# Kernel tuning notes

Measured on AMD Instinct MI355X. Metric: run time of the kernel, lower is better.

## Reference

```python
import jax, jax.numpy as jnp
import numpy as np

N_NODES, N_EDGES = 100000, 400000
D_NODE, D_EDGE, N_COND, N_ROUNDS = 128, 64, 2, 3


def gru_cell(x, h, Wih, Whh, bih, bhh):
    # Standard torch.nn.GRUCell math. x: [N, D] input, h: [N, D] hidden.
    gi = x @ Wih.T + bih            # [N, 3D]
    gh = h @ Whh.T + bhh            # [N, 3D]
    ir, iz, inn = jnp.split(gi, 3, axis=-1)
    hr, hz, hn = jnp.split(gh, 3, axis=-1)
    r = jax.nn.sigmoid(ir + hr)
    z = jax.nn.sigmoid(iz + hz)
    n = jnp.tanh(inn + r * hn)
    return (1.0 - z) * n + z * h


def setup_inputs() -> dict:
    key = jax.random.key(0)
    ks = jax.random.split(key, 10)
    scale = jnp.float32(0.05)
    d_in = 2 * D_NODE + D_EDGE + N_COND  # 322, matches enc_U Linear in_features
    h = jax.random.normal(ks[0], (N_NODES, D_NODE), jnp.float32)
    e = jax.random.normal(ks[1], (N_EDGES, D_EDGE), jnp.float32)
    src = jax.random.randint(ks[2], (N_EDGES,), 0, N_NODES)
    dst = jax.random.randint(ks[3], (N_EDGES,), 0, N_NODES)
    cond = jax.random.normal(ks[4], (N_COND,), jnp.float32)
    U_W = jax.random.normal(ks[5], (N_ROUNDS, D_NODE, d_in), jnp.float32) * scale
    U_b = jnp.zeros((N_ROUNDS, D_NODE), jnp.float32)
    Wih = jax.random.normal(ks[6], (N_ROUNDS, 3 * D_NODE, D_NODE), jnp.float32) * scale
    Whh = jax.random.normal(ks[7], (N_ROUNDS, 3 * D_NODE, D_NODE), jnp.float32) * scale
    bih = jnp.zeros((N_ROUNDS, 3 * D_NODE), jnp.float32)
    bhh = jnp.zeros((N_ROUNDS, 3 * D_NODE), jnp.float32)
    return dict(h=h, e=e, src=src, dst=dst, cond=cond,
                U_W=U_W, U_b=U_b, Wih=Wih, Whh=Whh, bih=bih, bhh=bhh)


def reference(h, e, src, dst, cond, U_W, U_b, Wih, Whh, bih, bhh):
    # GGM encode(): 3 rounds of gather-concat-Linear(enc_U)-segment_sum-GRUCell(enc_C).
    n_nodes = h.shape[0]
    n_edges = e.shape[0]
    cond_e = jnp.broadcast_to(cond, (n_edges, cond.shape[0]))
    for k in range(U_W.shape[0]):
        # per-edge message input: [h_v, h_w, e_vw, condition] -> [E, 2D+DE+NC]
        x = jnp.concatenate([h[dst], h[src], e, cond_e], axis=-1)
        msg = x @ U_W[k].T + U_b[k]                              # [E, D]
        agg = jax.ops.segment_sum(msg, dst, num_segments=n_nodes)  # [N, D]
        h = gru_cell(agg, h, Wih[k], Whh[k], bih[k], bhh[k])
    return h
```

## Files before the change

kernel.cpp:

```cpp
#include <hip/hip_runtime.h>
#include <hip/hip_bf16.h>
#include <hip/hip_fp16.h>


#define D_NODE 128
#define D_EDGE 64
#define D_IN   322
#define GRU3   384
#define ROWS_BLK 256
#define PA_STRIDE 328
#define PB_STRIDE 136

typedef _Float16 f16x8 __attribute__((ext_vector_type(8)));
typedef _Float16 f16x4 __attribute__((ext_vector_type(4)));
typedef _Float16 f16x2 __attribute__((ext_vector_type(2)));
typedef float    f32x4 __attribute__((ext_vector_type(4)));
typedef unsigned short u16x8 __attribute__((ext_vector_type(8)));

__device__ __forceinline__ f16x8 as_f16x8(u16x8 v) { return __builtin_bit_cast(f16x8, v); }
__device__ __forceinline__ float sigm_(float x) { return 1.f / (1.f + __expf(-x)); }
__device__ __forceinline__ float tanh_(float x) { return 1.f - 2.f / (__expf(2.f * x) + 1.f); }

__global__ void hist_k(const int* __restrict__ dst, int* __restrict__ cnt, int E) {
    int t = blockIdx.x * 256 + threadIdx.x;
    if (t < E) atomicAdd(&cnt[dst[t]], 1);
}

__global__ __launch_bounds__(256) void scan1_k(const int* __restrict__ cnt, int* __restrict__ row_ptr,
                                               int* __restrict__ blk_sums, int N) {
    __shared__ int s[256];
    const int t = threadIdx.x;
    const int base = blockIdx.x * 1024 + t * 4;
    int v0 = (base + 0 < N) ? cnt[base + 0] : 0;
    int v1 = (base + 1 < N) ? cnt[base + 1] : 0;
    int v2 = (base + 2 < N) ? cnt[base + 2] : 0;
    int v3 = (base + 3 < N) ? cnt[base + 3] : 0;
    const int tot = v0 + v1 + v2 + v3;
    s[t] = tot;
    __syncthreads();
    for (int off = 1; off < 256; off <<= 1) {
        int u = (t >= off) ? s[t - off] : 0;
        __syncthreads();
        s[t] += u;
        __syncthreads();
    }
    const int excl = s[t] - tot;
    if (base + 0 < N) row_ptr[base + 0] = excl;
    if (base + 1 < N) row_ptr[base + 1] = excl + v0;
    if (base + 2 < N) row_ptr[base + 2] = excl + v0 + v1;
    if (base + 3 < N) row_ptr[base + 3] = excl + v0 + v1 + v2;
    if (t == 255) blk_sums[blockIdx.x] = s[255];
}

__global__ __launch_bounds__(256) void scan2_k(int* __restrict__ blk_sums, int NB,
                                               int* __restrict__ row_ptr, int N, int E) {
    __shared__ int s[256];
    const int t = threadIdx.x;
    const int v = (t < NB) ? blk_sums[t] : 0;
    s[t] = v;
    __syncthreads();
    for (int off = 1; off < 256; off <<= 1) {
        int u = (t >= off) ? s[t - off] : 0;
        __syncthreads();
        s[t] += u;
        __syncthreads();
    }
    if (t < NB) blk_sums[t] = s[t] - v;
    if (t == 0) row_ptr[N] = E;
}

__global__ __launch_bounds__(256) void scan3_k(int* __restrict__ row_ptr, int* __restrict__ cursor,
                                               const int* __restrict__ blk_sums, int N) {
    const int off = blk_sums[blockIdx.x];
    const int base = blockIdx.x * 1024 + threadIdx.x * 4;
#pragma unroll
    for (int j = 0; j < 4; ++j) {
        const int i = base + j;
        if (i < N) {
            const int v = row_ptr[i] + off;
            row_ptr[i] = v;
            cursor[i] = v;
        }
    }
}

__global__ void scatter_k(const int* __restrict__ src, const int* __restrict__ dst,
                          int* __restrict__ cursor, int* __restrict__ csr_src,
                          int* __restrict__ csr_eid, int E) {
    int t = blockIdx.x * 256 + threadIdx.x;
    if (t < E) {
        int d = dst[t];
        int pos = atomicAdd(&cursor[d], 1);
        csr_src[pos] = src[t];
        csr_eid[pos] = t;
    }
}

__global__ __launch_bounds__(320) void cvt_uwp_k(const float* __restrict__ in, _Float16* __restrict__ out) {
    const int row = blockIdx.x;
    const int t = threadIdx.x;
    out[(size_t)row * 320 + t] = (_Float16)in[(size_t)row * D_IN + t];
}

__global__ void cvt_f32_k(const float* __restrict__ in, _Float16* __restrict__ out, int n) {
    int t = blockIdx.x * 256 + threadIdx.x;
    if (t < n) out[t] = (_Float16)in[t];
}

__global__ void cvt4_k(const float* __restrict__ in, _Float16* __restrict__ out, int n4) {
    int t = blockIdx.x * 256 + threadIdx.x;
    if (t < n4) {
        const f32x4 v = ((const f32x4*)in)[t];
        f16x4 r;
        r[0] = (_Float16)v[0]; r[1] = (_Float16)v[1];
        r[2] = (_Float16)v[2]; r[3] = (_Float16)v[3];
        ((f16x4*)out)[t] = r;
    }
}

__global__ void cvt_out_k(const _Float16* __restrict__ in, float* __restrict__ out, int n4) {
    int t = blockIdx.x * 256 + threadIdx.x;
    if (t < n4) {
        const f16x4 v = ((const f16x4*)in)[t];
        f32x4 r;
        r[0] = (float)v[0]; r[1] = (float)v[1];
        r[2] = (float)v[2]; r[3] = (float)v[3];
        ((f32x4*)out)[t] = r;
    }
}

__global__ void compute_c_k(const float* __restrict__ UW, const float* __restrict__ Ub,
                            const float* __restrict__ cond, float* __restrict__ cvec) {
    int t = threadIdx.x;
    if (t < 3 * D_NODE) {
        int k = t >> 7, i = t & 127;
        const float* u = UW + (size_t)k * D_NODE * D_IN + (size_t)i * D_IN + 320;
        cvec[t] = u[0] * cond[0] + u[1] * cond[1] + Ub[k * D_NODE + i];
    }
}

__global__ __launch_bounds__(256) void gather_e_k(const float* __restrict__ e,
                                                  const int* __restrict__ row_ptr,
                                                  const int* __restrict__ csr_eid,
                                                  _Float16* __restrict__ S_e, int N) {
    const int wave = threadIdx.x >> 6, lane = threadIdx.x & 63;
    const int n = blockIdx.x * 4 + wave;
    if (n >= N) return;
    const int p0 = row_ptr[n], p1 = row_ptr[n + 1];
    float a = 0.f, b = 0.f, c = 0.f, d = 0.f;
    int p = p0;
    for (; p + 3 < p1; p += 4) {
        const int e0 = csr_eid[p], e1 = csr_eid[p + 1], e2 = csr_eid[p + 2], e3 = csr_eid[p + 3];
        a += e[(size_t)e0 * D_EDGE + lane];
        b += e[(size_t)e1 * D_EDGE + lane];
        c += e[(size_t)e2 * D_EDGE + lane];
        d += e[(size_t)e3 * D_EDGE + lane];
    }
    for (; p < p1; ++p) a += e[(size_t)csr_eid[p] * D_EDGE + lane];
    S_e[(size_t)n * D_EDGE + lane] = (_Float16)((a + b) + (c + d));
}

__global__ __launch_bounds__(256) void gather_e16_k(const _Float16* __restrict__ e16,
                                                    const int* __restrict__ row_ptr,
                                                    const int* __restrict__ csr_eid,
                                                    _Float16* __restrict__ S_e, int N) {
    const int wave = threadIdx.x >> 6, lane = threadIdx.x & 63;
    const int half = lane >> 5, ln = lane & 31;
    const int n = blockIdx.x * 8 + wave * 2 + half;
    if (n >= N) return;
    const unsigned* ep = (const unsigned*)e16;
    const int p0 = row_ptr[n], p1 = row_ptr[n + 1];
    float a0 = 0.f, a1 = 0.f, b0 = 0.f, b1 = 0.f;
    float c0 = 0.f, c1 = 0.f, d0 = 0.f, d1 = 0.f;
    int p = p0;
    for (; p + 3 < p1; p += 4) {
        const int e0 = csr_eid[p], e1 = csr_eid[p + 1], e2 = csr_eid[p + 2], e3 = csr_eid[p + 3];
        const f16x2 v0 = __builtin_bit_cast(f16x2, ep[(size_t)e0 * 32 + ln]);
        const f16x2 v1 = __builtin_bit_cast(f16x2, ep[(size_t)e1 * 32 + ln]);
        const f16x2 v2 = __builtin_bit_cast(f16x2, ep[(size_t)e2 * 32 + ln]);
        const f16x2 v3 = __builtin_bit_cast(f16x2, ep[(size_t)e3 * 32 + ln]);
        a0 += (float)v0[0]; a1 += (float)v0[1];
        b0 += (float)v1[0]; b1 += (float)v1[1];
        c0 += (float)v2[0]; c1 += (float)v2[1];
        d0 += (float)v3[0]; d1 += (float)v3[1];
    }
    for (; p < p1; ++p) {
        const f16x2 v = __builtin_bit_cast(f16x2, ep[(size_t)csr_eid[p] * 32 + ln]);
        a0 += (float)v[0]; a1 += (float)v[1];
    }
    f16x2 r;
    r[0] = (_Float16)((a0 + b0) + (c0 + d0));
    r[1] = (_Float16)((a1 + b1) + (c1 + d1));
    ((unsigned*)S_e)[(size_t)n * 32 + ln] = __builtin_bit_cast(unsigned, r);
}

__global__ __launch_bounds__(256) void gather_h_k(const _Float16* __restrict__ h16,
                                                  const int* __restrict__ row_ptr,
                                                  const int* __restrict__ csr_src,
                                                  _Float16* __restrict__ S_h, int N) {
    const int wave = threadIdx.x >> 6, lane = threadIdx.x & 63;
    const int half = lane >> 5, ln = lane & 31;
    const int n = blockIdx.x * 8 + wave * 2 + half;
    if (n >= N) return;
    const uint2* hp = (const uint2*)h16;
    const int p0 = row_ptr[n], p1 = row_ptr[n + 1];
    float aA[4] = {0.f,0.f,0.f,0.f}, aB[4] = {0.f,0.f,0.f,0.f};
    float aC[4] = {0.f,0.f,0.f,0.f}, aD[4] = {0.f,0.f,0.f,0.f};
    int p = p0;
    for (; p + 3 < p1; p += 4) {
        const int s0 = csr_src[p], s1 = csr_src[p + 1], s2 = csr_src[p + 2], s3 = csr_src[p + 3];
        const f16x4 v0 = __builtin_bit_cast(f16x4, hp[(size_t)s0 * 32 + ln]);
        const f16x4 v1 = __builtin_bit_cast(f16x4, hp[(size_t)s1 * 32 + ln]);
        const f16x4 v2 = __builtin_bit_cast(f16x4, hp[(size_t)s2 * 32 + ln]);
        const f16x4 v3 = __builtin_bit_cast(f16x4, hp[(size_t)s3 * 32 + ln]);
#pragma unroll
        for (int j = 0; j < 4; ++j) {
            aA[j] += (float)v0[j]; aB[j] += (float)v1[j];
            aC[j] += (float)v2[j]; aD[j] += (float)v3[j];
        }
    }
    for (; p < p1; ++p) {
        const f16x4 v = __builtin_bit_cast(f16x4, hp[(size_t)csr_src[p] * 32 + ln]);
#pragma unroll
        for (int j = 0; j < 4; ++j) aA[j] += (float)v[j];
    }
    f16x4 r;
#pragma unroll
    for (int j = 0; j < 4; ++j) r[j] = (_Float16)((aA[j] + aB[j]) + (aC[j] + aD[j]));
    ((uint2*)S_h)[(size_t)n * 32 + ln] = __builtin_bit_cast(uint2, r);
}

__global__ __launch_bounds__(512, 2) void agg_k(
    const _Float16* __restrict__ h16,
    const _Float16* __restrict__ S_h,
    const _Float16* __restrict__ S_e,
    const int* __restrict__ row_ptr,
    const float* __restrict__ cvec,
    const _Float16* __restrict__ UWp,
    _Float16* __restrict__ agg,
    int N) {
    __shared__ __align__(16) _Float16 pbuf[2][16 * PA_STRIDE];

    const int tid  = threadIdx.x;
    const int wave = tid >> 6;
    const int lane = tid & 63;
    const int l15  = lane & 15;
    const int lg   = lane >> 4;
    const int rbase = blockIdx.x * ROWS_BLK + wave * 32;

    const unsigned short* hp  = (const unsigned short*)h16;
    const unsigned short* shp = (const unsigned short*)S_h;
    const unsigned short* sep = (const unsigned short*)S_e;
    const unsigned short* uwp = (const unsigned short*)UWp;

    f16x8 a_h[2][4], a_sh[2][4], a_se[2][2];
#pragma unroll
    for (int m = 0; m < 2; ++m) {
        const int arow = min(rbase + m * 16 + l15, N - 1);
#pragma unroll
        for (int kb = 0; kb < 4; ++kb) {
            a_h[m][kb]  = as_f16x8(*(const u16x8*)(hp  + (size_t)arow * D_NODE + kb * 32 + lg * 8));
            a_sh[m][kb] = as_f16x8(*(const u16x8*)(shp + (size_t)arow * D_NODE + kb * 32 + lg * 8));
        }
#pragma unroll
        for (int kb = 0; kb < 2; ++kb)
            a_se[m][kb] = as_f16x8(*(const u16x8*)(sep + (size_t)arow * D_EDGE + kb * 32 + lg * 8));
    }
    float degv[2][4];
#pragma unroll
    for (int m = 0; m < 2; ++m)
#pragma unroll
        for (int i = 0; i < 4; ++i) {
            const int n = min(rbase + m * 16 + lg * 4 + i, N - 1);
            degv[m][i] = (float)(row_ptr[n + 1] - row_ptr[n]);
        }

    u16x8 pr0, pr1;
    auto load_panel = [&](int nb) {
        const int c0 = tid, c1 = 512 + tid;
        pr0 = *(const u16x8*)(uwp + (size_t)(nb * 16 + c0 / 40) * 320 + (c0 % 40) * 8);
        if (c1 < 640)
            pr1 = *(const u16x8*)(uwp + (size_t)(nb * 16 + c1 / 40) * 320 + (c1 % 40) * 8);
    };
    auto write_panel = [&](int b) {
        const int c0 = tid, c1 = 512 + tid;
        *(u16x8*)&pbuf[b][(c0 / 40) * PA_STRIDE + (c0 % 40) * 8] = pr0;
        if (c1 < 640)
            *(u16x8*)&pbuf[b][(c1 / 40) * PA_STRIDE + (c1 % 40) * 8] = pr1;
    };

    load_panel(0);
    write_panel(0);
    __syncthreads();

#pragma unroll 1
    for (int nb = 0; nb < 8; ++nb) {
        if (nb < 7) load_panel(nb + 1);
        const _Float16* bp = pbuf[nb & 1];
        f32x4 acc1[2] = {{0.f,0.f,0.f,0.f},{0.f,0.f,0.f,0.f}};
        f32x4 acc2[2] = {{0.f,0.f,0.f,0.f},{0.f,0.f,0.f,0.f}};
#pragma unroll
        for (int kb = 0; kb < 10; ++kb) {
            f16x8 b = as_f16x8(*(const u16x8*)&bp[l15 * PA_STRIDE + kb * 32 + lg * 8]);
            if (kb < 4) {
                acc1[0] = __builtin_amdgcn_mfma_f32_16x16x32_f16(a_h[0][kb], b, acc1[0], 0, 0, 0);
                acc1[1] = __builtin_amdgcn_mfma_f32_16x16x32_f16(a_h[1][kb], b, acc1[1], 0, 0, 0);
            } else if (kb < 8) {
                acc2[0] = __builtin_amdgcn_mfma_f32_16x16x32_f16(a_sh[0][kb-4], b, acc2[0], 0, 0, 0);
                acc2[1] = __builtin_amdgcn_mfma_f32_16x16x32_f16(a_sh[1][kb-4], b, acc2[1], 0, 0, 0);
            } else {
                acc2[0] = __builtin_amdgcn_mfma_f32_16x16x32_f16(a_se[0][kb-8], b, acc2[0], 0, 0, 0);
                acc2[1] = __builtin_amdgcn_mfma_f32_16x16x32_f16(a_se[1][kb-8], b, acc2[1], 0, 0, 0);
            }
        }
        const float cv = cvec[nb * 16 + l15];
#pragma unroll
        for (int m = 0; m < 2; ++m)
#pragma unroll
            for (int i = 0; i < 4; ++i) {
                const int n = rbase + m * 16 + lg * 4 + i;
                if (n < N)
                    agg[(size_t)n * D_NODE + nb * 16 + l15] =
                        (_Float16)(degv[m][i] * (acc1[m][i] + cv) + acc2[m][i]);
            }
        if (nb < 7) write_panel((nb + 1) & 1);
        __syncthreads();
    }
}

__global__ __launch_bounds__(512, 2) void gru_k(
    _Float16* __restrict__ h16,
    const _Float16* __restrict__ agg,
    const _Float16* __restrict__ Wihh,
    const _Float16* __restrict__ Whhh,
    const float* __restrict__ bih,
    const float* __restrict__ bhh,
    int N) {
    __shared__ __align__(16) _Float16 pbuf[2][96 * PB_STRIDE];

    const int tid  = threadIdx.x;
    const int wave = tid >> 6;
    const int lane = tid & 63;
    const int l15  = lane & 15;
    const int lg   = lane >> 4;
    const int rbase = blockIdx.x * ROWS_BLK + wave * 32;

    const unsigned short* hp  = (const unsigned short*)h16;
    const unsigned short* agp = (const unsigned short*)agg;
    const unsigned short* wih = (const unsigned short*)Wihh;
    const unsigned short* whh = (const unsigned short*)Whhh;

    f16x8 a_ag[2][4], a_h[2][4];
#pragma unroll
    for (int m = 0; m < 2; ++m) {
        const int arow = min(rbase + m * 16 + l15, N - 1);
#pragma unroll
        for (int kb = 0; kb < 4; ++kb) {
            a_ag[m][kb] = as_f16x8(*(const u16x8*)(agp + (size_t)arow * D_NODE + kb * 32 + lg * 8));
            a_h[m][kb]  = as_f16x8(*(const u16x8*)(hp  + (size_t)arow * D_NODE + kb * 32 + lg * 8));
        }
    }

    u16x8 pr[3];
    auto load_panel = [&](int nb) {
#pragma unroll
        for (int r = 0; r < 3; ++r) {
            const int c = r * 512 + tid;
            const int row = c >> 4;
            const int off = (c & 15) * 8;
            const int gate = row >> 4;
            const int col = nb * 16 + (row & 15) + (gate % 3) * D_NODE;
            const unsigned short* mat = (gate < 3) ? wih : whh;
            pr[r] = *(const u16x8*)(mat + (size_t)col * D_NODE + off);
        }
    };
    auto write_panel = [&](int b) {
#pragma unroll
        for (int r = 0; r < 3; ++r) {
            const int c = r * 512 + tid;
            const int row = c >> 4;
            const int off = (c & 15) * 8;
            *(u16x8*)&pbuf[b][row * PB_STRIDE + off] = pr[r];
        }
    };

    load_panel(0);
    write_panel(0);
    __syncthreads();

#pragma unroll 1
    for (int nb = 0; nb < 8; ++nb) {
        if (nb < 7) load_panel(nb + 1);
        const int d = nb * 16 + l15;
        float hv[2][4];
#pragma unroll
        for (int m = 0; m < 2; ++m)
#pragma unroll
            for (int i = 0; i < 4; ++i) {
                const int n = min(rbase + m * 16 + lg * 4 + i, N - 1);
                hv[m][i] = (float)h16[(size_t)n * D_NODE + d];
            }
        const float bir = bih[d],       biz = bih[128 + d], bin = bih[256 + d];
        const float bhr = bhh[d],       bhz = bhh[128 + d], bhn = bhh[256 + d];

        const _Float16* bp = pbuf[nb & 1];
        f32x4 air[2] = {{0.f,0.f,0.f,0.f},{0.f,0.f,0.f,0.f}};
        f32x4 aiz[2] = {{0.f,0.f,0.f,0.f},{0.f,0.f,0.f,0.f}};
        f32x4 ain_[2] = {{0.f,0.f,0.f,0.f},{0.f,0.f,0.f,0.f}};
        f32x4 ahr[2] = {{0.f,0.f,0.f,0.f},{0.f,0.f,0.f,0.f}};
        f32x4 ahz[2] = {{0.f,0.f,0.f,0.f},{0.f,0.f,0.f,0.f}};
        f32x4 ahn[2] = {{0.f,0.f,0.f,0.f},{0.f,0.f,0.f,0.f}};
#pragma unroll
        for (int kb = 0; kb < 4; ++kb) {
            const int ko = kb * 32 + lg * 8;
            f16x8 b;
            b = as_f16x8(*(const u16x8*)&bp[(0 * 16 + l15) * PB_STRIDE + ko]);
            air[0] = __builtin_amdgcn_mfma_f32_16x16x32_f16(a_ag[0][kb], b, air[0], 0, 0, 0);
            air[1] = __builtin_amdgcn_mfma_f32_16x16x32_f16(a_ag[1][kb], b, air[1], 0, 0, 0);
            b = as_f16x8(*(const u16x8*)&bp[(1 * 16 + l15) * PB_STRIDE + ko]);
            aiz[0] = __builtin_amdgcn_mfma_f32_16x16x32_f16(a_ag[0][kb], b, aiz[0], 0, 0, 0);
            aiz[1] = __builtin_amdgcn_mfma_f32_16x16x32_f16(a_ag[1][kb], b, aiz[1], 0, 0, 0);
            b = as_f16x8(*(const u16x8*)&bp[(2 * 16 + l15) * PB_STRIDE + ko]);
            ain_[0] = __builtin_amdgcn_mfma_f32_16x16x32_f16(a_ag[0][kb], b, ain_[0], 0, 0, 0);
            ain_[1] = __builtin_amdgcn_mfma_f32_16x16x32_f16(a_ag[1][kb], b, ain_[1], 0, 0, 0);
            b = as_f16x8(*(const u16x8*)&bp[(3 * 16 + l15) * PB_STRIDE + ko]);
            ahr[0] = __builtin_amdgcn_mfma_f32_16x16x32_f16(a_h[0][kb], b, ahr[0], 0, 0, 0);
            ahr[1] = __builtin_amdgcn_mfma_f32_16x16x32_f16(a_h[1][kb], b, ahr[1], 0, 0, 0);
            b = as_f16x8(*(const u16x8*)&bp[(4 * 16 + l15) * PB_STRIDE + ko]);
            ahz[0] = __builtin_amdgcn_mfma_f32_16x16x32_f16(a_h[0][kb], b, ahz[0], 0, 0, 0);
            ahz[1] = __builtin_amdgcn_mfma_f32_16x16x32_f16(a_h[1][kb], b, ahz[1], 0, 0, 0);
            b = as_f16x8(*(const u16x8*)&bp[(5 * 16 + l15) * PB_STRIDE + ko]);
            ahn[0] = __builtin_amdgcn_mfma_f32_16x16x32_f16(a_h[0][kb], b, ahn[0], 0, 0, 0);
            ahn[1] = __builtin_amdgcn_mfma_f32_16x16x32_f16(a_h[1][kb], b, ahn[1], 0, 0, 0);
        }
#pragma unroll
        for (int m = 0; m < 2; ++m)
#pragma unroll
            for (int i = 0; i < 4; ++i) {
                const int n = rbase + m * 16 + lg * 4 + i;
                if (n < N) {
                    const float r  = sigm_(air[m][i] + bir + ahr[m][i] + bhr);
                    const float z  = sigm_(aiz[m][i] + biz + ahz[m][i] + bhz);
                    const float nn = tanh_(ain_[m][i] + bin + r * (ahn[m][i] + bhn));
                    h16[(size_t)n * D_NODE + d] = (_Float16)((1.f - z) * nn + z * hv[m][i]);
                }
            }
        if (nb < 7) write_panel((nb + 1) & 1);
        __syncthreads();
    }
}

extern "C" void kernel_launch(void* const* d_in, const int* in_sizes, int n_in,
                              void* d_out, int out_size, void* d_ws, size_t ws_size,
                              hipStream_t stream) {
    const float* h0   = (const float*)d_in[0];
    const float* e    = (const float*)d_in[1];
    const int*   src  = (const int*)d_in[2];
    const int*   dst  = (const int*)d_in[3];
    const float* cond = (const float*)d_in[4];
    const float* UW   = (const float*)d_in[5];
    const float* Ub   = (const float*)d_in[6];
    const float* Wih  = (const float*)d_in[7];
    const float* Whh  = (const float*)d_in[8];
    const float* bih  = (const float*)d_in[9];
    const float* bhh  = (const float*)d_in[10];

    const int N = in_sizes[0] / D_NODE;
    const int E = in_sizes[2];
    const int NB = (N + 1023) / 1024;
    const int NT = (N + ROWS_BLK - 1) / ROWS_BLK;

    char* wsb = (char*)d_ws;
    size_t off = 0;
    auto carve = [&](size_t bytes) -> char* {
        char* p = wsb + off;
        off = (off + bytes + 255) & ~(size_t)255;
        return p;
    };
    int*   cnt      = (int*)carve((size_t)N * 4);
    int*   row_ptr  = (int*)carve(((size_t)N + 1) * 4);
    int*   cursor   = (int*)carve((size_t)N * 4);
    int*   csr_src  = (int*)carve((size_t)E * 4);
    int*   csr_eid  = (int*)carve((size_t)E * 4);
    int*   blk_sums = (int*)carve(256 * 4);
    float* cvec     = (float*)carve(3 * D_NODE * 4);
    _Float16* S_e  = (_Float16*)carve((size_t)N * D_EDGE * 2);
    _Float16* S_h  = (_Float16*)carve((size_t)N * D_NODE * 2);
    _Float16* aggb = (_Float16*)carve((size_t)N * D_NODE * 2);
    _Float16* h16  = (_Float16*)carve((size_t)N * D_NODE * 2);
    _Float16* UWp  = (_Float16*)carve((size_t)3 * D_NODE * 320 * 2);
    _Float16* Wihh = (_Float16*)carve((size_t)3 * GRU3 * D_NODE * 2);
    _Float16* Whhh = (_Float16*)carve((size_t)3 * GRU3 * D_NODE * 2);
    const size_t e16_bytes = (size_t)E * D_EDGE * 2;
    _Float16* e16 = nullptr;
    if (off + e16_bytes + 256 <= ws_size) e16 = (_Float16*)carve(e16_bytes);
    (void)n_in; (void)out_size;

    hipMemsetAsync(cnt, 0, (size_t)N * 4, stream);
    hist_k<<<(E + 255) / 256, 256, 0, stream>>>(dst, cnt, E);
    scan1_k<<<NB, 256, 0, stream>>>(cnt, row_ptr, blk_sums, N);
    scan2_k<<<1, 256, 0, stream>>>(blk_sums, NB, row_ptr, N, E);
    scan3_k<<<NB, 256, 0, stream>>>(row_ptr, cursor, blk_sums, N);
    scatter_k<<<(E + 255) / 256, 256, 0, stream>>>(src, dst, cursor, csr_src, csr_eid, E);
    compute_c_k<<<1, 384, 0, stream>>>(UW, Ub, cond, cvec);
    cvt_uwp_k<<<3 * D_NODE, 320, 0, stream>>>(UW, UWp);
    {
        const int n1 = 3 * GRU3 * D_NODE;
        cvt_f32_k<<<(n1 + 255) / 256, 256, 0, stream>>>(Wih, Wihh, n1);
        cvt_f32_k<<<(n1 + 255) / 256, 256, 0, stream>>>(Whh, Whhh, n1);
    }
    {
        const int n4 = N * D_NODE / 4;
        cvt4_k<<<(n4 + 255) / 256, 256, 0, stream>>>(h0, h16, n4);
    }
    if (e16) {
        const int n4 = E * D_EDGE / 4;
        cvt4_k<<<(n4 + 255) / 256, 256, 0, stream>>>(e, e16, n4);
        gather_e16_k<<<(N + 7) / 8, 256, 0, stream>>>(e16, row_ptr, csr_eid, S_e, N);
    } else {
        gather_e_k<<<(N + 3) / 4, 256, 0, stream>>>(e, row_ptr, csr_eid, S_e, N);
    }

    for (int k = 0; k < 3; ++k) {
        gather_h_k<<<(N + 7) / 8, 256, 0, stream>>>(h16, row_ptr, csr_src, S_h, N);
        agg_k<<<NT, 512, 0, stream>>>(
            h16, S_h, S_e, row_ptr, cvec + k * D_NODE,
            UWp + (size_t)k * D_NODE * 320, aggb, N);
        gru_k<<<NT, 512, 0, stream>>>(
            h16, aggb,
            Wihh + (size_t)k * GRU3 * D_NODE,
            Whhh + (size_t)k * GRU3 * D_NODE,
            bih + (size_t)k * GRU3,
            bhh + (size_t)k * GRU3,
            N);
    }
    {
        const int n4 = N * D_NODE / 4;
        cvt_out_k<<<(n4 + 255) / 256, 256, 0, stream>>>(h16, (float*)d_out, n4);
    }
}
```

Measured before the change: 535.8 us.

## Keep weights in registers per wave; tile over rows instead of output panels

agg_k and gru_k switch from staging weight panels through double-buffered LDS to having each wave hold its 16-column slice of the weight matrices in registers. Each block then loops over 128 rows in 16-row chunks, re-reading activations for every wave. GRU output now goes to a separate ping-pong buffer, since different blocks/waves no longer own all columns of a row and in-place update would race. This removes the LDS traffic and barriers, but activations are now read once per wave (8x per block), and gru_k's launch bound drops to one block per CU because of register pressure.

```diff
diff --git a/kernel.cpp b/kernel.cpp
--- a/kernel.cpp
+++ b/kernel.cpp
@@ -7,7 +7,7 @@
 #define D_EDGE 64
 #define D_IN   322
 #define GRU3   384
-#define ROWS_BLK 256
+#define MROWS  128
 #define PA_STRIDE 328
 #define PB_STRIDE 136
 
@@ -231,7 +231,7 @@
 }
 
 __global__ __launch_bounds__(512, 2) void agg_k(
-    const _Float16* __restrict__ h16,
+    const _Float16* __restrict__ hcur,
     const _Float16* __restrict__ S_h,
     const _Float16* __restrict__ S_e,
     const int* __restrict__ row_ptr,
@@ -239,214 +239,141 @@
     const _Float16* __restrict__ UWp,
     _Float16* __restrict__ agg,
     int N) {
-    __shared__ __align__(16) _Float16 pbuf[2][16 * PA_STRIDE];
-
     const int tid  = threadIdx.x;
     const int wave = tid >> 6;
     const int lane = tid & 63;
     const int l15  = lane & 15;
     const int lg   = lane >> 4;
-    const int rbase = blockIdx.x * ROWS_BLK + wave * 32;
-
-    const unsigned short* hp  = (const unsigned short*)h16;
+    const int c0   = wave * 16 + l15;
+    const int row0 = blockIdx.x * MROWS;
+
+    const unsigned short* hp  = (const unsigned short*)hcur;
     const unsigned short* shp = (const unsigned short*)S_h;
     const unsigned short* sep = (const unsigned short*)S_e;
     const unsigned short* uwp = (const unsigned short*)UWp;
 
-    f16x8 a_h[2][4], a_sh[2][4], a_se[2][2];
-#pragma unroll
-    for (int m = 0; m < 2; ++m) {
-        const int arow = min(rbase + m * 16 + l15, N - 1);
+    f16x8 Bu[10];
+#pragma unroll
+    for (int kb = 0; kb < 10; ++kb)
+        Bu[kb] = as_f16x8(*(const u16x8*)(uwp + (size_t)c0 * 320 + kb * 32 + lg * 8));
+    const float cv = cvec[c0];
+
+#pragma unroll 1
+    for (int m = 0; m < MROWS / 16; ++m) {
+        const int r16 = row0 + m * 16;
+        const int arow = min(r16 + l15, N - 1);
+        f16x8 a_h[4], a_sh[4], a_se[2];
 #pragma unroll
         for (int kb = 0; kb < 4; ++kb) {
-            a_h[m][kb]  = as_f16x8(*(const u16x8*)(hp  + (size_t)arow * D_NODE + kb * 32 + lg * 8));
-            a_sh[m][kb] = as_f16x8(*(const u16x8*)(shp + (size_t)arow * D_NODE + kb * 32 + lg * 8));
+            a_h[kb]  = as_f16x8(*(const u16x8*)(hp  + (size_t)arow * D_NODE + kb * 32 + lg * 8));
+            a_sh[kb] = as_f16x8(*(const u16x8*)(shp + (size_t)arow * D_NODE + kb * 32 + lg * 8));
         }
 #pragma unroll
         for (int kb = 0; kb < 2; ++kb)
-            a_se[m][kb] = as_f16x8(*(const u16x8*)(sep + (size_t)arow * D_EDGE + kb * 32 + lg * 8));
-    }
-    float degv[2][4];
-#pragma unroll
-    for (int m = 0; m < 2; ++m)
+            a_se[kb] = as_f16x8(*(const u16x8*)(sep + (size_t)arow * D_EDGE + kb * 32 + lg * 8));
+        float degv[4];
 #pragma unroll
         for (int i = 0; i < 4; ++i) {
-            const int n = min(rbase + m * 16 + lg * 4 + i, N - 1);
-            degv[m][i] = (float)(row_ptr[n + 1] - row_ptr[n]);
-        }
-
-    u16x8 pr0, pr1;
-    auto load_panel = [&](int nb) {
-        const int c0 = tid, c1 = 512 + tid;
-        pr0 = *(const u16x8*)(uwp + (size_t)(nb * 16 + c0 / 40) * 320 + (c0 % 40) * 8);
-        if (c1 < 640)
-            pr1 = *(const u16x8*)(uwp + (size_t)(nb * 16 + c1 / 40) * 320 + (c1 % 40) * 8);
-    };
-    auto write_panel = [&](int b) {
-        const int c0 = tid, c1 = 512 + tid;
-        *(u16x8*)&pbuf[b][(c0 / 40) * PA_STRIDE + (c0 % 40) * 8] = pr0;
-        if (c1 < 640)
-            *(u16x8*)&pbuf[b][(c1 / 40) * PA_STRIDE + (c1 % 40) * 8] = pr1;
-    };
-
-    load_panel(0);
-    write_panel(0);
-    __syncthreads();
-
-#pragma unroll 1
-    for (int nb = 0; nb < 8; ++nb) {
-        if (nb < 7) load_panel(nb + 1);
-        const _Float16* bp = pbuf[nb & 1];
-        f32x4 acc1[2] = {{0.f,0.f,0.f,0.f},{0.f,0.f,0.f,0.f}};
-        f32x4 acc2[2] = {{0.f,0.f,0.f,0.f},{0.f,0.f,0.f,0.f}};
-#pragma unroll
-        for (int kb = 0; kb < 10; ++kb) {
-            f16x8 b = as_f16x8(*(const u16x8*)&bp[l15 * PA_STRIDE + kb * 32 + lg * 8]);
-            if (kb < 4) {
-                acc1[0] = __builtin_amdgcn_mfma_f32_16x16x32_f16(a_h[0][kb], b, acc1[0], 0, 0, 0);
-                acc1[1] = __builtin_amdgcn_mfma_f32_16x16x32_f16(a_h[1][kb], b, acc1[1], 0, 0, 0);
-            } else if (kb < 8) {
-                acc2[0] = __builtin_amdgcn_mfma_f32_16x16x32_f16(a_sh[0][kb-4], b, acc2[0], 0, 0, 0);
-                acc2[1] = __builtin_amdgcn_mfma_f32_16x16x32_f16(a_sh[1][kb-4], b, acc2[1], 0, 0, 0);
-            } else {
-                acc2[0] = __builtin_amdgcn_mfma_f32_16x16x32_f16(a_se[0][kb-8], b, acc2[0], 0, 0, 0);
-                acc2[1] = __builtin_amdgcn_mfma_f32_16x16x32_f16(a_se[1][kb-8], b, acc2[1], 0, 0, 0);
-            }
-        }
-        const float cv = cvec[nb * 16 + l15];
-#pragma unroll
-        for (int m = 0; m < 2; ++m)
-#pragma unroll
-            for (int i = 0; i < 4; ++i) {
-                const int n = rbase + m * 16 + lg * 4 + i;
-                if (n < N)
-                    agg[(size_t)n * D_NODE + nb * 16 + l15] =
-                        (_Float16)(degv[m][i] * (acc1[m][i] + cv) + acc2[m][i]);
-            }
-        if (nb < 7) write_panel((nb + 1) & 1);
-        __syncthreads();
-    }
-}
-
-__global__ __launch_bounds__(512, 2) void gru_k(
-    _Float16* __restrict__ h16,
+            const int n = min(r16 + lg * 4 + i, N - 1);
+            degv[i] = (float)(row_ptr[n + 1] - row_ptr[n]);
+        }
+
+        f32x4 acc1 = {0.f,0.f,0.f,0.f}, acc2 = {0.f,0.f,0.f,0.f};
+#pragma unroll
+        for (int kb = 0; kb < 4; ++kb)
+            acc1 = __builtin_amdgcn_mfma_f32_16x16x32_f16(a_h[kb], Bu[kb], acc1, 0, 0, 0);
+#pragma unroll
+        for (int kb = 0; kb < 4; ++kb)
+            acc2 = __builtin_amdgcn_mfma_f32_16x16x32_f16(a_sh[kb], Bu[4 + kb], acc2, 0, 0, 0);
+#pragma unroll
+        for (int kb = 0; kb < 2; ++kb)
+            acc2 = __builtin_amdgcn_mfma_f32_16x16x32_f16(a_se[kb], Bu[8 + kb], acc2, 0, 0, 0);
+
+#pragma unroll
+        for (int i = 0; i < 4; ++i) {
+            const int n = r16 + lg * 4 + i;
+            if (n < N)
+                agg[(size_t)n * D_NODE + c0] = (_Float16)(degv[i] * (acc1[i] + cv) + acc2[i]);
+        }
+    }
+}
+
+__global__ __launch_bounds__(512, 1) void gru_k(
+    const _Float16* __restrict__ hcur,
+    _Float16* __restrict__ hnext,
     const _Float16* __restrict__ agg,
     const _Float16* __restrict__ Wihh,
     const _Float16* __restrict__ Whhh,
     const float* __restrict__ bih,
     const float* __restrict__ bhh,
     int N) {
-    __shared__ __align__(16) _Float16 pbuf[2][96 * PB_STRIDE];
-
     const int tid  = threadIdx.x;
     const int wave = tid >> 6;
     const int lane = tid & 63;
     const int l15  = lane & 15;
     const int lg   = lane >> 4;
-    const int rbase = blockIdx.x * ROWS_BLK + wave * 32;
-
-    const unsigned short* hp  = (const unsigned short*)h16;
+    const int c0   = wave * 16 + l15;
+    const int row0 = blockIdx.x * MROWS;
+
+    const unsigned short* hp  = (const unsigned short*)hcur;
     const unsigned short* agp = (const unsigned short*)agg;
     const unsigned short* wih = (const unsigned short*)Wihh;
     const unsigned short* whh = (const unsigned short*)Whhh;
 
-    f16x8 a_ag[2][4], a_h[2][4];
-#pragma unroll
-    for (int m = 0; m < 2; ++m) {
-        const int arow = min(rbase + m * 16 + l15, N - 1);
+    f16x8 B[6][4];
+#pragma unroll
+    for (int g = 0; g < 3; ++g)
+#pragma unroll
+        for (int kb = 0; kb < 4; ++kb)
+            B[g][kb] = as_f16x8(*(const u16x8*)(wih + (size_t)(c0 + g * 128) * D_NODE + kb * 32 + lg * 8));
+#pragma unroll
+    for (int g = 0; g < 3; ++g)
+#pragma unroll
+        for (int kb = 0; kb < 4; ++kb)
+            B[3 + g][kb] = as_f16x8(*(const u16x8*)(whh + (size_t)(c0 + g * 128) * D_NODE + kb * 32 + lg * 8));
+
+    const float bir = bih[c0],       biz = bih[128 + c0], bin = bih[256 + c0];
+    const float bhr = bhh[c0],       bhz = bhh[128 + c0], bhn = bhh[256 + c0];
+
+#pragma unroll 1
+    for (int m = 0; m < MROWS / 16; ++m) {
+        const int r16 = row0 + m * 16;
+        const int arow = min(r16 + l15, N - 1);
+        f16x8 a_ag[4], a_h[4];
 #pragma unroll
         for (int kb = 0; kb < 4; ++kb) {
-            a_ag[m][kb] = as_f16x8(*(const u16x8*)(agp + (size_t)arow * D_NODE + kb * 32 + lg * 8));
-            a_h[m][kb]  = as_f16x8(*(const u16x8*)(hp  + (size_t)arow * D_NODE + kb * 32 + lg * 8));
-        }
-    }
-
-    u16x8 pr[3];
-    auto load_panel = [&](int nb) {
-#pragma unroll
-        for (int r = 0; r < 3; ++r) {
-            const int c = r * 512 + tid;
-            const int row = c >> 4;
-            const int off = (c & 15) * 8;
-            const int gate = row >> 4;
-            const int col = nb * 16 + (row & 15) + (gate % 3) * D_NODE;
-            const unsigned short* mat = (gate < 3) ? wih : whh;
-            pr[r] = *(const u16x8*)(mat + (size_t)col * D_NODE + off);
-        }
-    };
-    auto write_panel = [&](int b) {
-#pragma unroll
-        for (int r = 0; r < 3; ++r) {
-            const int c = r * 512 + tid;
-            const int row = c >> 4;
-            const int off = (c & 15) * 8;
-            *(u16x8*)&pbuf[b][row * PB_STRIDE + off] = pr[r];
-        }
-    };
-
-    load_panel(0);
-    write_panel(0);
-    __syncthreads();
-
-#pragma unroll 1
-    for (int nb = 0; nb < 8; ++nb) {
-        if (nb < 7) load_panel(nb + 1);
-        const int d = nb * 16 + l15;
-        float hv[2][4];
-#pragma unroll
-        for (int m = 0; m < 2; ++m)
-#pragma unroll
-            for (int i = 0; i < 4; ++i) {
-                const int n = min(rbase + m * 16 + lg * 4 + i, N - 1);
-                hv[m][i] = (float)h16[(size_t)n * D_NODE + d];
+            a_ag[kb] = as_f16x8(*(const u16x8*)(agp + (size_t)arow * D_NODE + kb * 32 + lg * 8));
+            a_h[kb]  = as_f16x8(*(const u16x8*)(hp  + (size_t)arow * D_NODE + kb * 32 + lg * 8));
+        }
+        float hv[4];
+#pragma unroll
+        for (int i = 0; i < 4; ++i) {
+            const int n = min(r16 + lg * 4 + i, N - 1);
+            hv[i] = (float)hcur[(size_t)n * D_NODE + c0];
+        }
+
+        f32x4 air = {0.f,0.f,0.f,0.f}, aiz = {0.f,0.f,0.f,0.f}, ain_ = {0.f,0.f,0.f,0.f};
+        f32x4 ahr = {0.f,0.f,0.f,0.f}, ahz = {0.f,0.f,0.f,0.f}, ahn = {0.f,0.f,0.f,0.f};
+#pragma unroll
+        for (int kb = 0; kb < 4; ++kb) {
+            air  = __builtin_amdgcn_mfma_f32_16x16x32_f16(a_ag[kb], B[0][kb], air, 0, 0, 0);
+            aiz  = __builtin_amdgcn_mfma_f32_16x16x32_f16(a_ag[kb], B[1][kb], aiz, 0, 0, 0);
+            ain_ = __builtin_amdgcn_mfma_f32_16x16x32_f16(a_ag[kb], B[2][kb], ain_, 0, 0, 0);
+            ahr  = __builtin_amdgcn_mfma_f32_16x16x32_f16(a_h[kb],  B[3][kb], ahr, 0, 0, 0);
+            ahz  = __builtin_amdgcn_mfma_f32_16x16x32_f16(a_h[kb],  B[4][kb], ahz, 0, 0, 0);
+            ahn  = __builtin_amdgcn_mfma_f32_16x16x32_f16(a_h[kb],  B[5][kb], ahn, 0, 0, 0);
+        }
+
+#pragma unroll
+        for (int i = 0; i < 4; ++i) {
+            const int n = r16 + lg * 4 + i;
+            if (n < N) {
+                const float r  = sigm_(air[i] + bir + ahr[i] + bhr);
+                const float z  = sigm_(aiz[i] + biz + ahz[i] + bhz);
+                const float nn = tanh_(ain_[i] + bin + r * (ahn[i] + bhn));
+                hnext[(size_t)n * D_NODE + c0] = (_Float16)((1.f - z) * nn + z * hv[i]);
             }
-        const float bir = bih[d],       biz = bih[128 + d], bin = bih[256 + d];
-        const float bhr = bhh[d],       bhz = bhh[128 + d], bhn = bhh[256 + d];
-
-        const _Float16* bp = pbuf[nb & 1];
-        f32x4 air[2] = {{0.f,0.f,0.f,0.f},{0.f,0.f,0.f,0.f}};
-        f32x4 aiz[2] = {{0.f,0.f,0.f,0.f},{0.f,0.f,0.f,0.f}};
-        f32x4 ain_[2] = {{0.f,0.f,0.f,0.f},{0.f,0.f,0.f,0.f}};
-        f32x4 ahr[2] = {{0.f,0.f,0.f,0.f},{0.f,0.f,0.f,0.f}};
-        f32x4 ahz[2] = {{0.f,0.f,0.f,0.f},{0.f,0.f,0.f,0.f}};
-        f32x4 ahn[2] = {{0.f,0.f,0.f,0.f},{0.f,0.f,0.f,0.f}};
-#pragma unroll
-        for (int kb = 0; kb < 4; ++kb) {
-            const int ko = kb * 32 + lg * 8;
-            f16x8 b;
-            b = as_f16x8(*(const u16x8*)&bp[(0 * 16 + l15) * PB_STRIDE + ko]);
-            air[0] = __builtin_amdgcn_mfma_f32_16x16x32_f16(a_ag[0][kb], b, air[0], 0, 0, 0);
-            air[1] = __builtin_amdgcn_mfma_f32_16x16x32_f16(a_ag[1][kb], b, air[1], 0, 0, 0);
-            b = as_f16x8(*(const u16x8*)&bp[(1 * 16 + l15) * PB_STRIDE + ko]);
-            aiz[0] = __builtin_amdgcn_mfma_f32_16x16x32_f16(a_ag[0][kb], b, aiz[0], 0, 0, 0);
-            aiz[1] = __builtin_amdgcn_mfma_f32_16x16x32_f16(a_ag[1][kb], b, aiz[1], 0, 0, 0);
-            b = as_f16x8(*(const u16x8*)&bp[(2 * 16 + l15) * PB_STRIDE + ko]);
-            ain_[0] = __builtin_amdgcn_mfma_f32_16x16x32_f16(a_ag[0][kb], b, ain_[0], 0, 0, 0);
-            ain_[1] = __builtin_amdgcn_mfma_f32_16x16x32_f16(a_ag[1][kb], b, ain_[1], 0, 0, 0);
-            b = as_f16x8(*(const u16x8*)&bp[(3 * 16 + l15) * PB_STRIDE + ko]);
-            ahr[0] = __builtin_amdgcn_mfma_f32_16x16x32_f16(a_h[0][kb], b, ahr[0], 0, 0, 0);
-            ahr[1] = __builtin_amdgcn_mfma_f32_16x16x32_f16(a_h[1][kb], b, ahr[1], 0, 0, 0);
-            b = as_f16x8(*(const u16x8*)&bp[(4 * 16 + l15) * PB_STRIDE + ko]);
-            ahz[0] = __builtin_amdgcn_mfma_f32_16x16x32_f16(a_h[0][kb], b, ahz[0], 0, 0, 0);
-            ahz[1] = __builtin_amdgcn_mfma_f32_16x16x32_f16(a_h[1][kb], b, ahz[1], 0, 0, 0);
-            b = as_f16x8(*(const u16x8*)&bp[(5 * 16 + l15) * PB_STRIDE + ko]);
-            ahn[0] = __builtin_amdgcn_mfma_f32_16x16x32_f16(a_h[0][kb], b, ahn[0], 0, 0, 0);
-            ahn[1] = __builtin_amdgcn_mfma_f32_16x16x32_f16(a_h[1][kb], b, ahn[1], 0, 0, 0);
-        }
-#pragma unroll
-        for (int m = 0; m < 2; ++m)
-#pragma unroll
-            for (int i = 0; i < 4; ++i) {
-                const int n = rbase + m * 16 + lg * 4 + i;
-                if (n < N) {
-                    const float r  = sigm_(air[m][i] + bir + ahr[m][i] + bhr);
-                    const float z  = sigm_(aiz[m][i] + biz + ahz[m][i] + bhz);
-                    const float nn = tanh_(ain_[m][i] + bin + r * (ahn[m][i] + bhn));
-                    h16[(size_t)n * D_NODE + d] = (_Float16)((1.f - z) * nn + z * hv[m][i]);
-                }
-            }
-        if (nb < 7) write_panel((nb + 1) & 1);
-        __syncthreads();
+        }
     }
 }
 
@@ -468,7 +395,7 @@
     const int N = in_sizes[0] / D_NODE;
     const int E = in_sizes[2];
     const int NB = (N + 1023) / 1024;
-    const int NT = (N + ROWS_BLK - 1) / ROWS_BLK;
+    const int NT = (N + MROWS - 1) / MROWS;
 
     char* wsb = (char*)d_ws;
     size_t off = 0;
@@ -487,7 +414,8 @@
     _Float16* S_e  = (_Float16*)carve((size_t)N * D_EDGE * 2);
     _Float16* S_h  = (_Float16*)carve((size_t)N * D_NODE * 2);
     _Float16* aggb = (_Float16*)carve((size_t)N * D_NODE * 2);
-    _Float16* h16  = (_Float16*)carve((size_t)N * D_NODE * 2);
+    _Float16* h16a = (_Float16*)carve((size_t)N * D_NODE * 2);
+    _Float16* h16b = (_Float16*)carve((size_t)N * D_NODE * 2);
     _Float16* UWp  = (_Float16*)carve((size_t)3 * D_NODE * 320 * 2);
     _Float16* Wihh = (_Float16*)carve((size_t)3 * GRU3 * D_NODE * 2);
     _Float16* Whhh = (_Float16*)carve((size_t)3 * GRU3 * D_NODE * 2);
@@ -511,7 +439,7 @@
     }
     {
         const int n4 = N * D_NODE / 4;
-        cvt4_k<<<(n4 + 255) / 256, 256, 0, stream>>>(h0, h16, n4);
+        cvt4_k<<<(n4 + 255) / 256, 256, 0, stream>>>(h0, h16a, n4);
     }
     if (e16) {
         const int n4 = E * D_EDGE / 4;
@@ -521,21 +449,24 @@
         gather_e_k<<<(N + 3) / 4, 256, 0, stream>>>(e, row_ptr, csr_eid, S_e, N);
     }
 
+    _Float16* hcur = h16a;
+    _Float16* hnext = h16b;
     for (int k = 0; k < 3; ++k) {
-        gather_h_k<<<(N + 7) / 8, 256, 0, stream>>>(h16, row_ptr, csr_src, S_h, N);
+        gather_h_k<<<(N + 7) / 8, 256, 0, stream>>>(hcur, row_ptr, csr_src, S_h, N);
         agg_k<<<NT, 512, 0, stream>>>(
-            h16, S_h, S_e, row_ptr, cvec + k * D_NODE,
+            hcur, S_h, S_e, row_ptr, cvec + k * D_NODE,
             UWp + (size_t)k * D_NODE * 320, aggb, N);
         gru_k<<<NT, 512, 0, stream>>>(
-            h16, aggb,
+            hcur, hnext, aggb,
             Wihh + (size_t)k * GRU3 * D_NODE,
             Whhh + (size_t)k * GRU3 * D_NODE,
             bih + (size_t)k * GRU3,
             bhh + (size_t)k * GRU3,
             N);
+        _Float16* t = hcur; hcur = hnext; hnext = t;
     }
     {
         const int n4 = N * D_NODE / 4;
-        cvt_out_k<<<(n4 + 255) / 256, 256, 0, stream>>>(h16, (float*)d_out, n4);
-    }
-}
+        cvt_out_k<<<(n4 + 255) / 256, 256, 0, stream>>>(hcur, (float*)d_out, n4);
+    }
+}
```

Measured after the change: 768.1 us. 43.4% more time.
